# Kernel optimization log

Hardware: AMD Instinct MI355X
Metric: run time of the kernel (lower is better)

Reference implementation:

```python
import jax, jax.numpy as jnp
import numpy as np

# DeformConv1d config (matches init_kwargs)
K = 3          # kernel_size
DIL = 1        # dilation
STRIDE = 1
PAD = DIL * (K - 1)  # 'same' total padding = 2 -> (1,1) reflect


def setup_inputs() -> dict:
    key = jax.random.key(0)
    k1, k2, k3, k4 = jax.random.split(key, 4)
    B, C, L = 16, 64, 8192
    O = 64
    x = jax.random.normal(k1, (B, C, L), dtype=jnp.float32)
    offsets = jax.random.normal(k2, (B, 1, L, K), dtype=jnp.float32)
    weight = jax.random.normal(k3, (O, C, K), dtype=jnp.float32) * (1.0 / np.sqrt(C * K))
    bias = jax.random.normal(k4, (O,), dtype=jnp.float32) * 0.01
    return {"x": x, "offsets": offsets, "weight": weight, "bias": bias}


def _deform_conv1d(x, offsets, weight, bias):
    # reflect 'same' padding: left = PAD//2, right = PAD - PAD//2
    left = PAD // 2
    x_pad = jnp.pad(x, ((0, 0), (0, 0), (left, PAD - left)), mode="reflect")
    B, C, Lp = x_pad.shape
    OL = offsets.shape[-2]
    dt = x.dtype

    dilated = (jnp.arange(K, dtype=dt) * DIL)          # [K] = [0, d, ..., d(K-1)]
    t0 = (jnp.arange(OL, dtype=dt) * STRIDE)[:, None]  # [OL, 1]

    # sampling positions T: [B, G, OL, K], constrained to kernel receptive field
    T = t0 + dilated + offsets
    T = jnp.maximum(T, t0)
    T = jnp.minimum(T, t0 + dilated[-1])

    # integer lower neighbors (no grad through floor); clamp so U+1 is valid
    U = jnp.clip(jnp.floor(T).astype(jnp.int32), 0, Lp - 2)  # [B, G, OL, K]

    # gather both neighbors along length axis (broadcast offset group -> C)
    idx = jnp.broadcast_to(U, (B, C, OL, K)).reshape(B, C, OL * K)
    x0 = jnp.take_along_axis(x_pad, idx, axis=2).reshape(B, C, OL, K)
    x1 = jnp.take_along_axis(x_pad, idx + 1, axis=2).reshape(B, C, OL, K)

    # linear interpolation weights G = max(0, 1 - |U - T|)
    Uf = U.astype(dt)
    w0 = jnp.maximum(0.0, 1.0 - jnp.abs(Uf - T))        # [B, G, OL, K]
    w1 = jnp.maximum(0.0, 1.0 - jnp.abs(Uf + 1.0 - T))
    sampled = w0 * x0 + w1 * x1                          # [B, C, OL, K]

    # conv1d(weight, stride=K) on flattened [B, C, OL*K] == per-position contraction
    out = jnp.einsum("bcok,fck->bfo", sampled, weight) + bias[None, :, None]
    return out


def reference(x, offsets, weight, bias):
    return _deform_conv1d(x, offsets, weight, bias)
```

## Files before the change

### kernel.cpp

```cpp
#include <hip/hip_runtime.h>
#include <hip/hip_bf16.h>
#include <stdint.h>

#define BB   16
#define CC   64
#define LL   8192
#define OO   64
#define KK   3
#define TT   64
#define XSW  68

typedef __attribute__((ext_vector_type(8))) short short8;
typedef __attribute__((ext_vector_type(4))) float float4_t;

__device__ __forceinline__ ushort f2bf(float f) {
    uint32_t u = __float_as_uint(f);
    return (ushort)((u + 0x7FFFu + ((u >> 16) & 1u)) >> 16);
}

__device__ __forceinline__ uint32_t pk2(float lo, float hi) {
    float2 t; t.x = lo; t.y = hi;
    __hip_bfloat162 h = __float22bfloat162_rn(t);
    return *(uint32_t*)&h;
}

__global__ void wt_prep(const float* __restrict__ w, ushort* __restrict__ wt) {
    int idx = blockIdx.x * 256 + threadIdx.x;
    if (idx < OO * CC * KK) {
        int f = idx / (CC * KK);
        int rem = idx - f * (CC * KK);
        int c = rem / KK;
        int k = rem - c * KK;
        wt[f * (KK * CC) + k * CC + c] = f2bf(w[idx]);
    }
}

__global__ __launch_bounds__(256, 6) void deform_main(
    const float* __restrict__ x, const float* __restrict__ offs,
    const ushort* __restrict__ wt, const float* __restrict__ bias,
    float* __restrict__ out) {

    __shared__ float xs[72 * XSW];

    const int tid  = threadIdx.x;
    const int bb   = blockIdx.x >> 7;
    const int tile = blockIdx.x & 127;
    const int ts   = tile * TT;
    const int lane = tid & 63;
    const int wv   = tid >> 6;

    {
        const float* xb = x + (size_t)bb * (CC * LL);
        const int c     = wv * 16 + (lane >> 2);
        const int fb    = lane & 3;
        const float* xrow = xb + (size_t)c * LL;
        #pragma unroll
        for (int i = 0; i < 5; i++) {
            int fi = fb + 4 * i;
            int j0 = ts - 4 + 4 * fi;
            if (fi < 18 && j0 >= 0 && j0 <= LL - 4) {
                float4 v = *(const float4*)(xrow + j0);
                float* dst = &xs[(4 * fi) * XSW + c];
                dst[0 * XSW] = v.x; dst[1 * XSW] = v.y;
                dst[2 * XSW] = v.z; dst[3 * XSW] = v.w;
            }
        }
        if (tile == 0   && tid < 64) xs[3 * XSW + tid]  = xb[(size_t)tid * LL + 1];
        if (tile == 127 && tid < 64) xs[68 * XSW + tid] = xb[(size_t)tid * LL + (LL - 2)];
    }

    const int lr = lane & 15;
    const int q  = lane >> 4;
    const int n  = wv * 16 + lr;
    int   ppk[KK];
    float w0k[KK], w1k[KK];
    {
        const float* ob = offs + ((size_t)bb * LL + ts + n) * KK;
        const float t0 = (float)(ts + n);
        #pragma unroll
        for (int k = 0; k < KK; k++) {
            float T = t0 + (float)k + ob[k];
            T = fmaxf(T, t0);
            T = fminf(T, t0 + 2.0f);
            int U = (int)floorf(T);
            if (U > LL) U = LL;
            float Uf = (float)U;
            ppk[k] = U - ts + 3;
            w0k[k] = fmaxf(0.0f, 1.0f - fabsf(Uf - T));
            w1k[k] = fmaxf(0.0f, 1.0f - fabsf(Uf + 1.0f - T));
        }
    }
    __syncthreads();

    float4_t acc0 = {0.f, 0.f, 0.f, 0.f};
    float4_t acc1 = acc0, acc2 = acc0, acc3 = acc0;

    #pragma unroll
    for (int kk = 0; kk < 6; kk++) {
        const int k0 = kk * 32 + q * 8;
        const int k  = k0 >> 6;
        const int c0 = k0 & 63;
        const int pp = ppk[k];
        const float w0 = w0k[k], w1 = w1k[k];
        const float4 r0a = *(const float4*)&xs[pp * XSW + c0];
        const float4 r0b = *(const float4*)&xs[pp * XSW + c0 + 4];
        const float4 r1a = *(const float4*)&xs[(pp + 1) * XSW + c0];
        const float4 r1b = *(const float4*)&xs[(pp + 1) * XSW + c0 + 4];
        union { short8 s; uint32_t u32[4]; } af;
        af.u32[0] = pk2(w0 * r0a.x + w1 * r1a.x, w0 * r0a.y + w1 * r1a.y);
        af.u32[1] = pk2(w0 * r0a.z + w1 * r1a.z, w0 * r0a.w + w1 * r1a.w);
        af.u32[2] = pk2(w0 * r0b.x + w1 * r1b.x, w0 * r0b.y + w1 * r1b.y);
        af.u32[3] = pk2(w0 * r0b.z + w1 * r1b.z, w0 * r0b.w + w1 * r1b.w);
        short8 b0 = *(const short8*)&wt[(0 * 16 + lr) * (KK * CC) + k0];
        short8 b1 = *(const short8*)&wt[(1 * 16 + lr) * (KK * CC) + k0];
        short8 b2 = *(const short8*)&wt[(2 * 16 + lr) * (KK * CC) + k0];
        short8 b3 = *(const short8*)&wt[(3 * 16 + lr) * (KK * CC) + k0];
        acc0 = __builtin_amdgcn_mfma_f32_16x16x32_bf16(af.s, b0, acc0, 0, 0, 0);
        acc1 = __builtin_amdgcn_mfma_f32_16x16x32_bf16(af.s, b1, acc1, 0, 0, 0);
        acc2 = __builtin_amdgcn_mfma_f32_16x16x32_bf16(af.s, b2, acc2, 0, 0, 0);
        acc3 = __builtin_amdgcn_mfma_f32_16x16x32_bf16(af.s, b3, acc3, 0, 0, 0);
    }

    const int pos0 = ts + wv * 16 + q * 4;
    float4_t accs[4] = {acc0, acc1, acc2, acc3};
    #pragma unroll
    for (int ft = 0; ft < 4; ft++) {
        const int f = ft * 16 + lr;
        const float bv = bias[f];
        float4 o;
        o.x = accs[ft][0] + bv;
        o.y = accs[ft][1] + bv;
        o.z = accs[ft][2] + bv;
        o.w = accs[ft][3] + bv;
        *(float4*)(out + ((size_t)bb * OO + f) * LL + pos0) = o;
    }
}

extern "C" void kernel_launch(void* const* d_in, const int* in_sizes, int n_in,
                              void* d_out, int out_size, void* d_ws, size_t ws_size,
                              hipStream_t stream) {
    const float* x    = (const float*)d_in[0];
    const float* offs = (const float*)d_in[1];
    const float* w    = (const float*)d_in[2];
    const float* bias = (const float*)d_in[3];
    float* out = (float*)d_out;
    ushort* wt = (ushort*)d_ws;

    hipLaunchKernelGGL(wt_prep, dim3((OO * CC * KK + 255) / 256), dim3(256), 0, stream, w, wt);
    hipLaunchKernelGGL(deform_main, dim3(BB * (LL / TT)), dim3(256), 0, stream,
                       x, offs, wt, bias, out);
}
```

Measured before the change: 116.7 us.

## Persistent blocks with double-buffered bf16 LDS tiles and register-resident weights

The kernel now launches 768 persistent blocks that each process 2–3 tiles in sequence. The next tile's x and offsets are prefetched into registers while the current tile computes, then staged as bf16 into the alternate LDS buffer. Weights and bias are loaded into registers once per block rather than once per tile. Storing x in bf16 halves LDS traffic and footprint, but x is now rounded to bf16 before interpolation, and the larger register budget lowers the occupancy target to 3 blocks per CU.

New measurement: 108.6 us. 1.08x faster.

```diff
diff --git a/kernel.cpp b/kernel.cpp
--- a/kernel.cpp
+++ b/kernel.cpp
@@ -8,7 +8,7 @@
 #define OO   64
 #define KK   3
 #define TT   64
-#define XSW  68
+#define XSW  72
 
 typedef __attribute__((ext_vector_type(8))) short short8;
 typedef __attribute__((ext_vector_type(4))) float float4_t;
@@ -17,7 +17,9 @@
     uint32_t u = __float_as_uint(f);
     return (ushort)((u + 0x7FFFu + ((u >> 16) & 1u)) >> 16);
 }
-
+__device__ __forceinline__ float bf2f(ushort h) {
+    return __uint_as_float(((uint32_t)h) << 16);
+}
 __device__ __forceinline__ uint32_t pk2(float lo, float hi) {
     float2 t; t.x = lo; t.y = hi;
     __hip_bfloat162 h = __float22bfloat162_rn(t);
@@ -35,104 +37,147 @@
     }
 }
 
-__global__ __launch_bounds__(256, 6) void deform_main(
+__global__ __launch_bounds__(256, 3) void deform_main(
     const float* __restrict__ x, const float* __restrict__ offs,
     const ushort* __restrict__ wt, const float* __restrict__ bias,
     float* __restrict__ out) {
 
-    __shared__ float xs[72 * XSW];
+    __shared__ ushort xs[2][72 * XSW];
 
     const int tid  = threadIdx.x;
-    const int bb   = blockIdx.x >> 7;
-    const int tile = blockIdx.x & 127;
-    const int ts   = tile * TT;
     const int lane = tid & 63;
     const int wv   = tid >> 6;
+    const int lr   = lane & 15;
+    const int q    = lane >> 4;
+    const int g    = blockIdx.x;
 
-    {
-        const float* xb = x + (size_t)bb * (CC * LL);
-        const int c     = wv * 16 + (lane >> 2);
-        const int fb    = lane & 3;
-        const float* xrow = xb + (size_t)c * LL;
+    int t0, cnt;
+    if (g < 512) { t0 = 3 * g; cnt = 3; }
+    else         { t0 = 2 * g + 512; cnt = 2; }
+
+    short8 br[6][4];
+    #pragma unroll
+    for (int kk = 0; kk < 6; kk++)
+        #pragma unroll
+        for (int ft = 0; ft < 4; ft++)
+            br[kk][ft] = *(const short8*)&wt[(ft * 16 + lr) * (KK * CC) + kk * 32 + q * 8];
+    float bv[4];
+    #pragma unroll
+    for (int ft = 0; ft < 4; ft++) bv[ft] = bias[ft * 16 + lr];
+
+    const int cch = wv * 16 + (lane >> 2);
+    const int fb  = lane & 3;
+    const int n   = wv * 16 + lr;
+
+    float4 pv[5];
+    float  po[3];
+    int    ppk[3]; float w0k[3], w1k[3];
+
+    auto prefetch = [&](int tau) {
+        int bb = tau >> 7, ts = (tau & 127) * TT;
+        const float* xrow = x + ((size_t)bb * CC + cch) * LL;
+        #pragma unroll
+        for (int i = 0; i < 5; i++) {
+            int fi = fb + 4 * i;
+            int j0 = ts - 4 + 4 * fi;
+            if (fi < 18 && j0 >= 0 && j0 <= LL - 4)
+                pv[i] = *(const float4*)(xrow + j0);
+        }
+        const float* ob = offs + ((size_t)bb * LL + ts + n) * KK;
+        #pragma unroll
+        for (int k = 0; k < 3; k++) po[k] = ob[k];
+    };
+
+    auto stage = [&](int buf, int tau) {
+        int bb = tau >> 7, tile = tau & 127, ts = tile * TT;
+        ushort* xsb = xs[buf];
         #pragma unroll
         for (int i = 0; i < 5; i++) {
             int fi = fb + 4 * i;
             int j0 = ts - 4 + 4 * fi;
             if (fi < 18 && j0 >= 0 && j0 <= LL - 4) {
-                float4 v = *(const float4*)(xrow + j0);
-                float* dst = &xs[(4 * fi) * XSW + c];
-                dst[0 * XSW] = v.x; dst[1 * XSW] = v.y;
-                dst[2 * XSW] = v.z; dst[3 * XSW] = v.w;
+                ushort* d = &xsb[(4 * fi) * XSW + cch];
+                d[0 * XSW] = f2bf(pv[i].x); d[1 * XSW] = f2bf(pv[i].y);
+                d[2 * XSW] = f2bf(pv[i].z); d[3 * XSW] = f2bf(pv[i].w);
             }
         }
-        if (tile == 0   && tid < 64) xs[3 * XSW + tid]  = xb[(size_t)tid * LL + 1];
-        if (tile == 127 && tid < 64) xs[68 * XSW + tid] = xb[(size_t)tid * LL + (LL - 2)];
-    }
+        if (tile == 0   && tid < 64) xsb[ 3 * XSW + tid] = f2bf(x[((size_t)bb * CC + tid) * LL + 1]);
+        if (tile == 127 && tid < 64) xsb[68 * XSW + tid] = f2bf(x[((size_t)bb * CC + tid) * LL + (LL - 2)]);
+    };
 
-    const int lr = lane & 15;
-    const int q  = lane >> 4;
-    const int n  = wv * 16 + lr;
-    int   ppk[KK];
-    float w0k[KK], w1k[KK];
-    {
-        const float* ob = offs + ((size_t)bb * LL + ts + n) * KK;
-        const float t0 = (float)(ts + n);
+    auto uw = [&](int tau) {
+        int ts = (tau & 127) * TT;
+        float t0f = (float)(ts + n);
         #pragma unroll
-        for (int k = 0; k < KK; k++) {
-            float T = t0 + (float)k + ob[k];
-            T = fmaxf(T, t0);
-            T = fminf(T, t0 + 2.0f);
+        for (int k = 0; k < 3; k++) {
+            float T = t0f + (float)k + po[k];
+            T = fmaxf(T, t0f);
+            T = fminf(T, t0f + 2.0f);
             int U = (int)floorf(T);
             if (U > LL) U = LL;
             float Uf = (float)U;
             ppk[k] = U - ts + 3;
-            w0k[k] = fmaxf(0.0f, 1.0f - fabsf(Uf - T));
-            w1k[k] = fmaxf(0.0f, 1.0f - fabsf(Uf + 1.0f - T));
+            w0k[k] = fmaxf(0.f, 1.f - fabsf(Uf - T));
+            w1k[k] = fmaxf(0.f, 1.f - fabsf(Uf + 1.f - T));
         }
-    }
+    };
+
+    prefetch(t0);
+    stage(0, t0);
+    uw(t0);
     __syncthreads();
 
-    float4_t acc0 = {0.f, 0.f, 0.f, 0.f};
-    float4_t acc1 = acc0, acc2 = acc0, acc3 = acc0;
+    for (int it = 0; it < cnt; ++it) {
+        const int tau = t0 + it;
+        const int bb = tau >> 7, ts = (tau & 127) * TT;
+        const bool more = (it + 1 < cnt);
+        if (more) prefetch(tau + 1);
 
-    #pragma unroll
-    for (int kk = 0; kk < 6; kk++) {
-        const int k0 = kk * 32 + q * 8;
-        const int k  = k0 >> 6;
-        const int c0 = k0 & 63;
-        const int pp = ppk[k];
-        const float w0 = w0k[k], w1 = w1k[k];
-        const float4 r0a = *(const float4*)&xs[pp * XSW + c0];
-        const float4 r0b = *(const float4*)&xs[pp * XSW + c0 + 4];
-        const float4 r1a = *(const float4*)&xs[(pp + 1) * XSW + c0];
-        const float4 r1b = *(const float4*)&xs[(pp + 1) * XSW + c0 + 4];
-        union { short8 s; uint32_t u32[4]; } af;
-        af.u32[0] = pk2(w0 * r0a.x + w1 * r1a.x, w0 * r0a.y + w1 * r1a.y);
-        af.u32[1] = pk2(w0 * r0a.z + w1 * r1a.z, w0 * r0a.w + w1 * r1a.w);
-        af.u32[2] = pk2(w0 * r0b.x + w1 * r1b.x, w0 * r0b.y + w1 * r1b.y);
-        af.u32[3] = pk2(w0 * r0b.z + w1 * r1b.z, w0 * r0b.w + w1 * r1b.w);
-        short8 b0 = *(const short8*)&wt[(0 * 16 + lr) * (KK * CC) + k0];
-        short8 b1 = *(const short8*)&wt[(1 * 16 + lr) * (KK * CC) + k0];
-        short8 b2 = *(const short8*)&wt[(2 * 16 + lr) * (KK * CC) + k0];
-        short8 b3 = *(const short8*)&wt[(3 * 16 + lr) * (KK * CC) + k0];
-        acc0 = __builtin_amdgcn_mfma_f32_16x16x32_bf16(af.s, b0, acc0, 0, 0, 0);
-        acc1 = __builtin_amdgcn_mfma_f32_16x16x32_bf16(af.s, b1, acc1, 0, 0, 0);
-        acc2 = __builtin_amdgcn_mfma_f32_16x16x32_bf16(af.s, b2, acc2, 0, 0, 0);
-        acc3 = __builtin_amdgcn_mfma_f32_16x16x32_bf16(af.s, b3, acc3, 0, 0, 0);
-    }
+        const ushort* xsb = xs[it & 1];
+        float4_t acc0 = {0.f, 0.f, 0.f, 0.f};
+        float4_t acc1 = acc0, acc2 = acc0, acc3 = acc0;
 
-    const int pos0 = ts + wv * 16 + q * 4;
-    float4_t accs[4] = {acc0, acc1, acc2, acc3};
-    #pragma unroll
-    for (int ft = 0; ft < 4; ft++) {
-        const int f = ft * 16 + lr;
-        const float bv = bias[f];
-        float4 o;
-        o.x = accs[ft][0] + bv;
-        o.y = accs[ft][1] + bv;
-        o.z = accs[ft][2] + bv;
-        o.w = accs[ft][3] + bv;
-        *(float4*)(out + ((size_t)bb * OO + f) * LL + pos0) = o;
+        #pragma unroll
+        for (int kk = 0; kk < 6; kk++) {
+            const int k0 = kk * 32 + q * 8;
+            const int k  = k0 >> 6;
+            const int c0 = k0 & 63;
+            const int pp = ppk[k];
+            const float w0 = w0k[k], w1 = w1k[k];
+            union { uint4 v; ushort u16[8]; } r0, r1;
+            r0.v = *(const uint4*)&xsb[pp * XSW + c0];
+            r1.v = *(const uint4*)&xsb[(pp + 1) * XSW + c0];
+            union { short8 s; uint32_t u32[4]; } af;
+            #pragma unroll
+            for (int j = 0; j < 4; j++) {
+                float v0 = w0 * bf2f(r0.u16[2 * j])     + w1 * bf2f(r1.u16[2 * j]);
+                float v1 = w0 * bf2f(r0.u16[2 * j + 1]) + w1 * bf2f(r1.u16[2 * j + 1]);
+                af.u32[j] = pk2(v0, v1);
+            }
+            acc0 = __builtin_amdgcn_mfma_f32_16x16x32_bf16(af.s, br[kk][0], acc0, 0, 0, 0);
+            acc1 = __builtin_amdgcn_mfma_f32_16x16x32_bf16(af.s, br[kk][1], acc1, 0, 0, 0);
+            acc2 = __builtin_amdgcn_mfma_f32_16x16x32_bf16(af.s, br[kk][2], acc2, 0, 0, 0);
+            acc3 = __builtin_amdgcn_mfma_f32_16x16x32_bf16(af.s, br[kk][3], acc3, 0, 0, 0);
+        }
+
+        const int pos0 = ts + wv * 16 + q * 4;
+        float4_t accs[4] = {acc0, acc1, acc2, acc3};
+        #pragma unroll
+        for (int ft = 0; ft < 4; ft++) {
+            const int f = ft * 16 + lr;
+            float4 o;
+            o.x = accs[ft][0] + bv[ft];
+            o.y = accs[ft][1] + bv[ft];
+            o.z = accs[ft][2] + bv[ft];
+            o.w = accs[ft][3] + bv[ft];
+            *(float4*)(out + ((size_t)bb * OO + f) * LL + pos0) = o;
+        }
+
+        if (more) {
+            stage((it + 1) & 1, tau + 1);
+            uw(tau + 1);
+            __syncthreads();
+        }
     }
 }
 
@@ -147,6 +192,6 @@
     ushort* wt = (ushort*)d_ws;
 
     hipLaunchKernelGGL(wt_prep, dim3((OO * CC * KK + 255) / 256), dim3(256), 0, stream, w, wt);
-    hipLaunchKernelGGL(deform_main, dim3(BB * (LL / TT)), dim3(256), 0, stream,
+    hipLaunchKernelGGL(deform_main, dim3(768), dim3(256), 0, stream,
                        x, offs, wt, bias, out);
 }
```

## Replace shared-memory x tile staging with direct per-lane global gathers

Applied to the files above, without the earlier changes.

Removes the LDS tile of x and the block barrier. Each wave now handles an independent 16-position chunk and gathers the two interpolation neighbours straight from global memory, with reflect padding folded into the index math. This avoids the LDS transpose-store traffic and the __syncthreads, but turns the x reads into strided scalar loads across channels that depend on caches for coalescing. The launch-bounds occupancy hint drops from 6 to 3, which may free registers for the larger set of loads in flight.

Result: slower. 121.8 us (+4.3%).

```diff
diff --git a/kernel.cpp b/kernel.cpp
--- a/kernel.cpp
+++ b/kernel.cpp
@@ -7,8 +7,6 @@
 #define LL   8192
 #define OO   64
 #define KK   3
-#define TT   64
-#define XSW  68
 
 typedef __attribute__((ext_vector_type(8))) short short8;
 typedef __attribute__((ext_vector_type(4))) float float4_t;
@@ -17,7 +15,6 @@
     uint32_t u = __float_as_uint(f);
     return (ushort)((u + 0x7FFFu + ((u >> 16) & 1u)) >> 16);
 }
-
 __device__ __forceinline__ uint32_t pk2(float lo, float hi) {
     float2 t; t.x = lo; t.y = hi;
     __hip_bfloat162 h = __float22bfloat162_rn(t);
@@ -35,48 +32,28 @@
     }
 }
 
-__global__ __launch_bounds__(256, 6) void deform_main(
+__global__ __launch_bounds__(256, 3) void deform_main(
     const float* __restrict__ x, const float* __restrict__ offs,
     const ushort* __restrict__ wt, const float* __restrict__ bias,
     float* __restrict__ out) {
 
-    __shared__ float xs[72 * XSW];
+    const int tid   = threadIdx.x;
+    const int lane  = tid & 63;
+    const int wv    = tid >> 6;
+    const int lr    = lane & 15;
+    const int q     = lane >> 4;
+    const int chunk = blockIdx.x * 4 + wv;
+    const int bb    = chunk >> 9;
+    const int pos0  = (chunk & 511) * 16;
+    const int n     = pos0 + lr;
 
-    const int tid  = threadIdx.x;
-    const int bb   = blockIdx.x >> 7;
-    const int tile = blockIdx.x & 127;
-    const int ts   = tile * TT;
-    const int lane = tid & 63;
-    const int wv   = tid >> 6;
+    const float* xb = x + (size_t)bb * (CC * LL);
 
-    {
-        const float* xb = x + (size_t)bb * (CC * LL);
-        const int c     = wv * 16 + (lane >> 2);
-        const int fb    = lane & 3;
-        const float* xrow = xb + (size_t)c * LL;
-        #pragma unroll
-        for (int i = 0; i < 5; i++) {
-            int fi = fb + 4 * i;
-            int j0 = ts - 4 + 4 * fi;
-            if (fi < 18 && j0 >= 0 && j0 <= LL - 4) {
-                float4 v = *(const float4*)(xrow + j0);
-                float* dst = &xs[(4 * fi) * XSW + c];
-                dst[0 * XSW] = v.x; dst[1 * XSW] = v.y;
-                dst[2 * XSW] = v.z; dst[3 * XSW] = v.w;
-            }
-        }
-        if (tile == 0   && tid < 64) xs[3 * XSW + tid]  = xb[(size_t)tid * LL + 1];
-        if (tile == 127 && tid < 64) xs[68 * XSW + tid] = xb[(size_t)tid * LL + (LL - 2)];
-    }
-
-    const int lr = lane & 15;
-    const int q  = lane >> 4;
-    const int n  = wv * 16 + lr;
-    int   ppk[KK];
+    int   j0k[KK], j1k[KK];
     float w0k[KK], w1k[KK];
     {
-        const float* ob = offs + ((size_t)bb * LL + ts + n) * KK;
-        const float t0 = (float)(ts + n);
+        const float* ob = offs + ((size_t)bb * LL + n) * KK;
+        const float t0 = (float)n;
         #pragma unroll
         for (int k = 0; k < KK; k++) {
             float T = t0 + (float)k + ob[k];
@@ -85,43 +62,48 @@
             int U = (int)floorf(T);
             if (U > LL) U = LL;
             float Uf = (float)U;
-            ppk[k] = U - ts + 3;
-            w0k[k] = fmaxf(0.0f, 1.0f - fabsf(Uf - T));
-            w1k[k] = fmaxf(0.0f, 1.0f - fabsf(Uf + 1.0f - T));
+            w0k[k] = fmaxf(0.f, 1.f - fabsf(Uf - T));
+            w1k[k] = fmaxf(0.f, 1.f - fabsf(Uf + 1.f - T));
+            int a = U - 1;  j0k[k] = (a < 0) ? 1 : a;
+            j1k[k] = (U <= LL - 1) ? U : (LL - 2);
         }
     }
-    __syncthreads();
 
     float4_t acc0 = {0.f, 0.f, 0.f, 0.f};
     float4_t acc1 = acc0, acc2 = acc0, acc3 = acc0;
 
     #pragma unroll
     for (int kk = 0; kk < 6; kk++) {
-        const int k0 = kk * 32 + q * 8;
-        const int k  = k0 >> 6;
-        const int c0 = k0 & 63;
-        const int pp = ppk[k];
+        const int k  = kk >> 1;
+        const int c0 = (kk & 1) * 32 + q * 8;
+        const float* p0 = xb + (size_t)c0 * LL + j0k[k];
+        const float* p1 = xb + (size_t)c0 * LL + j1k[k];
+        float xv0[8], xv1[8];
+        #pragma unroll
+        for (int cc = 0; cc < 8; cc++) {
+            xv0[cc] = p0[(size_t)cc * LL];
+            xv1[cc] = p1[(size_t)cc * LL];
+        }
         const float w0 = w0k[k], w1 = w1k[k];
-        const float4 r0a = *(const float4*)&xs[pp * XSW + c0];
-        const float4 r0b = *(const float4*)&xs[pp * XSW + c0 + 4];
-        const float4 r1a = *(const float4*)&xs[(pp + 1) * XSW + c0];
-        const float4 r1b = *(const float4*)&xs[(pp + 1) * XSW + c0 + 4];
         union { short8 s; uint32_t u32[4]; } af;
-        af.u32[0] = pk2(w0 * r0a.x + w1 * r1a.x, w0 * r0a.y + w1 * r1a.y);
-        af.u32[1] = pk2(w0 * r0a.z + w1 * r1a.z, w0 * r0a.w + w1 * r1a.w);
-        af.u32[2] = pk2(w0 * r0b.x + w1 * r1b.x, w0 * r0b.y + w1 * r1b.y);
-        af.u32[3] = pk2(w0 * r0b.z + w1 * r1b.z, w0 * r0b.w + w1 * r1b.w);
-        short8 b0 = *(const short8*)&wt[(0 * 16 + lr) * (KK * CC) + k0];
-        short8 b1 = *(const short8*)&wt[(1 * 16 + lr) * (KK * CC) + k0];
-        short8 b2 = *(const short8*)&wt[(2 * 16 + lr) * (KK * CC) + k0];
-        short8 b3 = *(const short8*)&wt[(3 * 16 + lr) * (KK * CC) + k0];
+        #pragma unroll
+        for (int j = 0; j < 4; j++) {
+            float v0 = w0 * xv0[2 * j]     + w1 * xv1[2 * j];
+            float v1 = w0 * xv0[2 * j + 1] + w1 * xv1[2 * j + 1];
+            af.u32[j] = pk2(v0, v1);
+        }
+        const ushort* wrow = wt + kk * 32 + q * 8;
+        short8 b0 = *(const short8*)&wrow[(0 * 16 + lr) * (KK * CC)];
+        short8 b1 = *(const short8*)&wrow[(1 * 16 + lr) * (KK * CC)];
+        short8 b2 = *(const short8*)&wrow[(2 * 16 + lr) * (KK * CC)];
+        short8 b3 = *(const short8*)&wrow[(3 * 16 + lr) * (KK * CC)];
         acc0 = __builtin_amdgcn_mfma_f32_16x16x32_bf16(af.s, b0, acc0, 0, 0, 0);
         acc1 = __builtin_amdgcn_mfma_f32_16x16x32_bf16(af.s, b1, acc1, 0, 0, 0);
         acc2 = __builtin_amdgcn_mfma_f32_16x16x32_bf16(af.s, b2, acc2, 0, 0, 0);
         acc3 = __builtin_amdgcn_mfma_f32_16x16x32_bf16(af.s, b3, acc3, 0, 0, 0);
     }
 
-    const int pos0 = ts + wv * 16 + q * 4;
+    const int posq = pos0 + q * 4;
     float4_t accs[4] = {acc0, acc1, acc2, acc3};
     #pragma unroll
     for (int ft = 0; ft < 4; ft++) {
@@ -132,7 +114,7 @@
         o.y = accs[ft][1] + bv;
         o.z = accs[ft][2] + bv;
         o.w = accs[ft][3] + bv;
-        *(float4*)(out + ((size_t)bb * OO + f) * LL + pos0) = o;
+        *(float4*)(out + ((size_t)bb * OO + f) * LL + posq) = o;
     }
 }
 
@@ -147,6 +129,6 @@
     ushort* wt = (ushort*)d_ws;
 
     hipLaunchKernelGGL(wt_prep, dim3((OO * CC * KK + 255) / 256), dim3(256), 0, stream, w, wt);
-    hipLaunchKernelGGL(deform_main, dim3(BB * (LL / TT)), dim3(256), 0, stream,
+    hipLaunchKernelGGL(deform_main, dim3(2048), dim3(256), 0, stream,
                        x, offs, wt, bias, out);
 }
```
